# Optimization experiments

Measured on AMD Instinct MI355X. Metric: run time of the kernel, lower is better.

## Reference

```python
import jax, jax.numpy as jnp
import numpy as np

PAD, BOS, EOS, UNK = 0, 1, 2, 3
B, S, V, D, L = 256, 512, 50000, 256, 128

def setup_inputs() -> dict:
    key = jax.random.key(0)
    ks = jax.random.split(key, 12)
    vocab_tensor = jax.random.randint(ks[0], (B, S), 4, V)
    parent_idx = jax.random.randint(ks[1], (B, S), 0, S)
    pbond = jax.random.randint(ks[2], (B, S), 0, 4)
    bond = jax.random.randint(ks[3], (B, S), 0, 4)
    patom = jax.random.randint(ks[4], (B, S), 0, 16)
    atom = jax.random.randint(ks[5], (B, S), 0, 16)
    btype = jax.random.randint(ks[6], (B, S), 0, 4)
    order_tensor = jnp.stack([parent_idx, pbond, bond, patom, atom, btype], axis=-1)
    lengths = jax.random.randint(ks[7], (B,), 1, S + 1)
    mask_tensor = jnp.arange(S)[None, :] < lengths[:, None]  # ragged prefix masks
    eps = jax.random.normal(ks[8], (B, L), dtype=jnp.float32)
    sc = 1.0 / np.sqrt(D)
    emb = jax.random.normal(ks[9], (V, D), dtype=jnp.float32) * sc
    Wm = jax.random.normal(ks[10], (D, L), dtype=jnp.float32) * sc
    Wv = jax.random.normal(ks[11], (D, L), dtype=jnp.float32) * sc
    Wlin = jax.random.normal(jax.random.fold_in(key, 20), (L, D), dtype=jnp.float32) / np.sqrt(L)
    Wout = jax.random.normal(jax.random.fold_in(key, 21), (D, D), dtype=jnp.float32) * sc
    return {
        'vocab_tensor': vocab_tensor, 'order_tensor': order_tensor, 'mask_tensor': mask_tensor,
        'eps': eps, 'emb': emb, 'Wm': Wm, 'bm': jnp.zeros((L,), jnp.float32),
        'Wv': Wv, 'bv': jnp.zeros((L,), jnp.float32), 'Wlin': Wlin,
        'blin': jnp.zeros((D,), jnp.float32), 'Wout': Wout, 'bout': jnp.zeros((D,), jnp.float32),
    }

def _forward(vocab_tensor, order_tensor, mask_tensor, eps, emb, Wm, bm, Wv, bv, Wlin, blin, Wout, bout):
    # --- mask bond-pos columns (torch.where assignments, vectorized) ---
    # (columns 1 and 2 set to -1 where masked; kept implicitly via vt/pad handling)
    # --- calc_chem_z path: masked vocab, parent gather, edge one-hot ---
    vt = jnp.where(mask_tensor, vocab_tensor, PAD)                      # [B,S]
    vocab_emb = emb[vt]                                                 # [B,S,D]
    oi = order_tensor[..., 0]
    oi = jnp.where(oi == -1, BOS, oi)
    parent = jnp.where(mask_tensor, jnp.take_along_axis(vt, oi, axis=1), PAD)
    parent = parent.at[:, 0].set(BOS)
    parent_emb = emb[parent]                                            # [B,S,D]
    idx = jnp.clip(order_tensor[..., 5] - 1, -1, None)
    edge_type = jnp.where((idx >= 0)[..., None],
                          jax.nn.one_hot(jnp.clip(idx, 0), 3, dtype=jnp.float32), 0.0)  # [B,S,3]
    # pooling stand-in for (undefined) StructureEncoder -> [B,D]
    m = mask_tensor[..., None].astype(jnp.float32)
    enc = ((vocab_emb + parent_emb) * m).sum(1) / jnp.maximum(m.sum(1), 1.0)
    enc = enc * (1.0 + 0.0 * edge_type.sum())  # keep edge_type in graph
    # --- LatentSampler ---
    mean = enc @ Wm + bm
    log_var = enc @ Wv + bv
    z = mean + eps * jnp.exp(0.5 * log_var)
    memory = z @ Wlin + blin                                            # [B,D]
    # --- vectorized bos/eos/pad sequence assembly (the hot loop in torch) ---
    inp = jnp.concatenate([jnp.full((B, 1), BOS, vocab_tensor.dtype), vocab_tensor], axis=1)  # [B,S+1]
    mask_ex = jnp.concatenate([jnp.ones((B, 1), bool), mask_tensor], axis=1)
    tgt = jnp.roll(inp, -1, axis=1)
    first_false = jnp.argmax(~mask_ex, axis=1)                          # first eos position
    has_false = jnp.any(~mask_ex, axis=1)
    pos = jnp.arange(S + 1)[None, :]
    tgt = jnp.where(has_false[:, None] & (pos == first_false[:, None] - 1), EOS, tgt)
    kill = has_false[:, None] & (pos >= first_false[:, None])
    tgt = jnp.where(kill, PAD, tgt)
    inp = jnp.where(kill, PAD, inp)
    # edge_index assembly (faithful, consumed by decoder in original)
    padneg = jnp.full((B, 1), -1, order_tensor.dtype)
    edge_index = jnp.concatenate([padneg, jnp.where(mask_tensor, order_tensor[..., 0], -2) + 1], axis=1)
    # --- embedding lookups + decoder stand-in + output head ---
    node_embed = emb[inp]                                               # [B,S+1,D]
    dec = node_embed + memory[:, None, :]
    dec = dec + 0.0 * edge_index[..., None].astype(jnp.float32)         # keep edge_index in graph
    word_emb = dec @ Wout + bout
    tgt_emb = emb[tgt]
    valid = (tgt != PAD)
    sq = (word_emb - tgt_emb) ** 2 * valid[..., None]
    token_loss = sq.sum() / jnp.maximum(valid.sum() * D, 1).astype(jnp.float32)
    kl = -0.5 * jnp.sum(1.0 + log_var - mean ** 2 - jnp.exp(log_var)) / B
    return token_loss, kl

def reference(vocab_tensor, order_tensor, mask_tensor, eps, emb, Wm, bm, Wv, bv, Wlin, blin, Wout, bout):
    return _forward(vocab_tensor, order_tensor, mask_tensor, eps, emb, Wm, bm, Wv, bv, Wlin, blin, Wout, bout)
```

## Files before the change

kernel.cpp:

```cpp
#include <hip/hip_runtime.h>

#define B_ 256
#define S_ 512
#define V_ 50000
#define D_ 256
#define L_ 128
#define NPK 64
#define NSP2 4
#define NLB (B_ * NSP2)

typedef __attribute__((ext_vector_type(8))) short short8;
typedef __attribute__((ext_vector_type(4))) float floatx4;

#define OFF_SQP 16
#define OFF_KL  (OFF_SQP + NLB)
#define OFF_CNT (OFF_KL + 256)
#define OFF_Q   (OFF_CNT + 256)
#define OFF_WB  (OFF_Q + B_ * D_)

__device__ __forceinline__ unsigned short f2bf(float x) {
    unsigned u = __float_as_uint(x);
    u += 0x7FFFu + ((u >> 16) & 1u);
    return (unsigned short)(u >> 16);
}
__device__ __forceinline__ float bf2f(unsigned short u) {
    return __uint_as_float(((unsigned)u) << 16);
}

__global__ __launch_bounds__(256) void enc1(
    const int* __restrict__ vocab, const int* __restrict__ order,
    const int* __restrict__ mask, const float* __restrict__ emb,
    const float* __restrict__ eps, const float* __restrict__ Wm,
    const float* __restrict__ bm, const float* __restrict__ Wv,
    const float* __restrict__ bv, const float* __restrict__ Wlin,
    const float* __restrict__ blin, const float* __restrict__ Wout,
    const float* __restrict__ bout, float* __restrict__ ws) {
    __shared__ __align__(16) char smem[11904];
    const int tid = threadIdx.x;
    if (blockIdx.x < NPK) {
        unsigned short* __restrict__ Wb = (unsigned short*)(ws + OFF_WB);
        const int t = blockIdx.x * 256 + tid;
        const int idx0 = t * 4;
        const int kk = idx0 >> 13;
        const int col = (idx0 >> 5) & 255;
        const int hi = (idx0 >> 3) & 3;
        const int e0 = idx0 & 7;
        const int kbase = kk * 32 + hi * 8 + e0;
        ushort4 h;
        h.x = f2bf(Wout[(size_t)(kbase + 0) * D_ + col]);
        h.y = f2bf(Wout[(size_t)(kbase + 1) * D_ + col]);
        h.z = f2bf(Wout[(size_t)(kbase + 2) * D_ + col]);
        h.w = f2bf(Wout[(size_t)(kbase + 3) * D_ + col]);
        ((ushort4*)Wb)[t] = h;
        return;
    }
    int* s_id1 = (int*)smem;
    int* s_id2 = s_id1 + S_;
    float4* s_part = (float4*)(smem + 4096);
    float* s_enc = (float*)(smem + 7168);
    float* s_mean = (float*)(smem + 8192);
    float* s_lv = (float*)(smem + 8704);
    float* s_z = (float*)(smem + 9216);
    float* s_mem = (float*)(smem + 9728);
    float* s_red = (float*)(smem + 10752);
    int* s_cntp = (int*)(smem + 11776);
    const int b = blockIdx.x - NPK;
    if (tid == 0) *s_cntp = 0;
    __syncthreads();
    for (int j = tid; j < S_; j += 256) {
        const int mk = mask[b * S_ + j];
        int id1 = 0, id2 = 0;
        if (mk) {
            id1 = vocab[b * S_ + j];
            if (j == 0) {
                id2 = 1;
            } else {
                int oi = order[(size_t)(b * S_ + j) * 6];
                if (oi == -1) oi = 1;
                id2 = mask[b * S_ + oi] ? vocab[b * S_ + oi] : 0;
            }
        }
        s_id1[j] = id1;
        s_id2[j] = id2;
        unsigned long long bal = __ballot(mk != 0);
        if ((tid & 63) == 0) atomicAdd(s_cntp, __popcll(bal));
    }
    __syncthreads();
    const int cnt = *s_cntp;
    const int jg = tid >> 6, d4 = tid & 63;
    const float4* eb4 = (const float4*)emb;
    float4 a = {0.f, 0.f, 0.f, 0.f};
#pragma unroll 4
    for (int j = jg; j < cnt; j += 4) {
        float4 x = eb4[(size_t)s_id1[j] * 64 + d4];
        float4 y = eb4[(size_t)s_id2[j] * 64 + d4];
        a.x += x.x + y.x; a.y += x.y + y.y;
        a.z += x.z + y.z; a.w += x.w + y.w;
    }
    if (jg) s_part[(jg - 1) * 64 + d4] = a;
    __syncthreads();
    if (jg == 0) {
#pragma unroll
        for (int g = 0; g < 3; ++g) {
            float4 p = s_part[g * 64 + d4];
            a.x += p.x; a.y += p.y; a.z += p.z; a.w += p.w;
        }
        const float inv = 1.f / fmaxf((float)cnt, 1.f);
        a.x *= inv; a.y *= inv; a.z *= inv; a.w *= inv;
        ((float4*)s_enc)[d4] = a;
    }
    __syncthreads();
    {
        const int l = tid & (L_ - 1);
        const float* W = (tid < L_) ? Wm : Wv;
        const float* bb = (tid < L_) ? bm : bv;
        float dot = bb[l];
        for (int d = 0; d < D_; ++d) dot = fmaf(s_enc[d], W[d * L_ + l], dot);
        if (tid < L_) s_mean[l] = dot; else s_lv[l] = dot;
    }
    __syncthreads();
    float klp = 0.f;
    if (tid < L_) {
        float mn = s_mean[tid], lv = s_lv[tid];
        s_z[tid] = mn + eps[b * L_ + tid] * expf(0.5f * lv);
        klp = 1.f + lv - mn * mn - expf(lv);
    }
    s_red[tid] = klp;
    __syncthreads();
    for (int s = 128; s > 0; s >>= 1) {
        if (tid < s) s_red[tid] += s_red[tid + s];
        __syncthreads();
    }
    if (tid == 0) {
        ws[OFF_KL + b] = s_red[0];
        ((int*)ws)[OFF_CNT + b] = cnt;
    }
    {
        float mem = blin[tid];
        for (int l2 = 0; l2 < L_; ++l2) mem = fmaf(s_z[l2], Wlin[l2 * D_ + tid], mem);
        s_mem[tid] = mem;
    }
    __syncthreads();
    {
        float qv = bout[tid];
        for (int k = 0; k < D_; ++k) qv = fmaf(s_mem[k], Wout[k * D_ + tid], qv);
        ws[OFF_Q + b * D_ + tid] = qv;
    }
}

__global__ __launch_bounds__(256, 2) void loss2(const int* __restrict__ vocab,
                                                const float* __restrict__ emb,
                                                float* __restrict__ ws) {
    __shared__ __align__(16) char smemA[8192];
    __shared__ __align__(16) float smemT[16 * 260];
    __shared__ int s_tgt[16];
    __shared__ float s_w[16];
    __shared__ int s_inp0;
    __shared__ float s_q[256];
    __shared__ float s_wred[4];
    const int tid = threadIdx.x;
    const int b = blockIdx.x >> 2, part = blockIdx.x & 3;
    const int lane = tid & 63, wv = tid >> 6;
    const int lo = lane & 15, hi = lane >> 4;
    const unsigned short* __restrict__ Wb = (const unsigned short*)(ws + OFF_WB);
    const int cnt = ((const int*)ws)[OFF_CNT + b];
    const int ntiles = (cnt + 16) >> 4;
    s_q[tid] = ws[OFF_Q + b * D_ + tid];
    short8 bfr[4][8];
#pragma unroll
    for (int nt = 0; nt < 4; ++nt)
#pragma unroll
        for (int kk = 0; kk < 8; ++kk)
            bfr[nt][kk] = *(const short8*)(Wb + kk * 8192 +
                                           (wv * 64 + nt * 16 + lo) * 32 + hi * 8);
    float sqacc = 0.f;
    for (int ti = part; ti < ntiles; ti += NSP2) {
        if (tid < 16) {
            const int j = ti * 16 + tid;
            s_tgt[tid] = (j < cnt) ? vocab[b * S_ + j] : ((cnt < S_) ? 2 : 1);
            s_w[tid] = (j <= cnt) ? 1.f : 0.f;
            if (tid == 0) s_inp0 = (ti == 0) ? 1 : vocab[b * S_ + ti * 16 - 1];
        }
        __syncthreads();
#pragma unroll
        for (int i = 0; i < 4; ++i) {
            const int fi = i * 256 + tid;
            const int row = fi >> 6, cf4 = fi & 63;
            float4 t = *((const float4*)(emb + (size_t)s_tgt[row] * D_) + cf4);
            *(float4*)(&smemT[row * 260 + cf4 * 4]) = t;
            if (row < 15) {
                const int arow = row + 1;
                ushort4 h;
                h.x = f2bf(t.x); h.y = f2bf(t.y); h.z = f2bf(t.z); h.w = f2bf(t.w);
                const int byt = (arow * 512 + cf4 * 8) ^ ((arow & 7) << 4);
                *(ushort4*)(smemA + byt) = h;
            }
        }
        if (tid < 64) {
            float4 v = *((const float4*)(emb + (size_t)s_inp0 * D_) + tid);
            ushort4 h;
            h.x = f2bf(v.x); h.y = f2bf(v.y); h.z = f2bf(v.z); h.w = f2bf(v.w);
            *(ushort4*)(smemA + tid * 8) = h;
        }
        __syncthreads();
        floatx4 acc[4];
#pragma unroll
        for (int nt = 0; nt < 4; ++nt) acc[nt] = (floatx4){0.f, 0.f, 0.f, 0.f};
#pragma unroll
        for (int kk = 0; kk < 8; ++kk) {
            const int byt = (lo * 512 + hi * 16 + kk * 64) ^ ((lo & 7) << 4);
            short8 av = *(const short8*)(smemA + byt);
#pragma unroll
            for (int nt = 0; nt < 4; ++nt)
                acc[nt] = __builtin_amdgcn_mfma_f32_16x16x32_bf16(
                    av, bfr[nt][kk], acc[nt], 0, 0, 0);
        }
#pragma unroll
        for (int nt = 0; nt < 4; ++nt) {
            const int col = wv * 64 + nt * 16 + lo;
            const float qv = s_q[col];
#pragma unroll
            for (int r = 0; r < 4; ++r) {
                const int row = hi * 4 + r;
                const float t = smemT[row * 260 + col];
                const float d = acc[nt][r] + qv - t;
                sqacc = fmaf(s_w[row] * d, d, sqacc);
            }
        }
        __syncthreads();
    }
#pragma unroll
    for (int off = 32; off; off >>= 1) sqacc += __shfl_down(sqacc, off, 64);
    if (lane == 0) s_wred[wv] = sqacc;
    __syncthreads();
    if (tid == 0)
        ws[OFF_SQP + blockIdx.x] = s_wred[0] + s_wred[1] + s_wred[2] + s_wred[3];
}

__global__ __launch_bounds__(256) void finalize3(const float* __restrict__ ws,
                                                 float* __restrict__ out) {
    __shared__ float s_red[256];
    const int tid = threadIdx.x;
    float sq = 0.f;
#pragma unroll
    for (int i = 0; i < NSP2; ++i) sq += ws[OFF_SQP + i * 256 + tid];
    s_red[tid] = sq;
    __syncthreads();
    for (int s = 128; s > 0; s >>= 1) {
        if (tid < s) s_red[tid] += s_red[tid + s];
        __syncthreads();
    }
    const float sq_tot = s_red[0];
    __syncthreads();
    s_red[tid] = ws[OFF_KL + tid];
    __syncthreads();
    for (int s = 128; s > 0; s >>= 1) {
        if (tid < s) s_red[tid] += s_red[tid + s];
        __syncthreads();
    }
    const float kl_tot = s_red[0];
    __syncthreads();
    s_red[tid] = (float)(((const int*)ws)[OFF_CNT + tid] + 1);
    __syncthreads();
    for (int s = 128; s > 0; s >>= 1) {
        if (tid < s) s_red[tid] += s_red[tid + s];
        __syncthreads();
    }
    if (tid == 0) {
        float denom = s_red[0] * (float)D_;
        if (denom < 1.f) denom = 1.f;
        out[0] = sq_tot / denom;
        out[1] = -0.5f * kl_tot / (float)B_;
    }
}

extern "C" void kernel_launch(void* const* d_in, const int* in_sizes, int n_in,
                              void* d_out, int out_size, void* d_ws, size_t ws_size,
                              hipStream_t stream) {
    const int* vocab = (const int*)d_in[0];
    const int* order = (const int*)d_in[1];
    const int* mask  = (const int*)d_in[2];
    const float* eps  = (const float*)d_in[3];
    const float* emb  = (const float*)d_in[4];
    const float* Wm   = (const float*)d_in[5];
    const float* bm   = (const float*)d_in[6];
    const float* Wv   = (const float*)d_in[7];
    const float* bv   = (const float*)d_in[8];
    const float* Wlin = (const float*)d_in[9];
    const float* blin = (const float*)d_in[10];
    const float* Wout = (const float*)d_in[11];
    const float* bout = (const float*)d_in[12];

    float* ws = (float*)d_ws;
    enc1<<<NPK + B_, 256, 0, stream>>>(vocab, order, mask, emb, eps, Wm, bm,
                                       Wv, bv, Wlin, blin, Wout, bout, ws);
    loss2<<<NLB, 256, 0, stream>>>(vocab, emb, ws);
    finalize3<<<1, 256, 0, stream>>>(ws, (float*)d_out);
}
```

Before: 181.9 us.

## Prefetch next tile's embeddings into registers and split tiles contiguously per block

Each block now takes a contiguous range of tiles instead of a strided one, and loads that range's vocab ids into shared memory once. While the MFMA work runs on the current tile, the embedding rows for the next tile are loaded into registers, which hides global gather latency behind compute. The row weights are computed inline and one barrier per iteration is dropped. The grid mapping is also reordered so that consecutive blocks belong to different batches, not to the same batch. The register prefetch raises register pressure under launch bounds of 2 blocks per SM.

```diff
diff --git a/kernel.cpp b/kernel.cpp
--- a/kernel.cpp
+++ b/kernel.cpp
@@ -153,18 +153,28 @@
                                                 float* __restrict__ ws) {
     __shared__ __align__(16) char smemA[8192];
     __shared__ __align__(16) float smemT[16 * 260];
-    __shared__ int s_tgt[16];
-    __shared__ float s_w[16];
-    __shared__ int s_inp0;
+    __shared__ int s_sid[160];
     __shared__ float s_q[256];
     __shared__ float s_wred[4];
     const int tid = threadIdx.x;
-    const int b = blockIdx.x >> 2, part = blockIdx.x & 3;
+    const int b = blockIdx.x & (B_ - 1), part = blockIdx.x >> 8;
     const int lane = tid & 63, wv = tid >> 6;
     const int lo = lane & 15, hi = lane >> 4;
     const unsigned short* __restrict__ Wb = (const unsigned short*)(ws + OFF_WB);
     const int cnt = ((const int*)ws)[OFF_CNT + b];
     const int ntiles = (cnt + 16) >> 4;
+    const int per16 = (ntiles + NSP2 - 1) / NSP2;
+    const int tb = part * per16;
+    const int te = min(tb + per16, ntiles);
+    if (tb >= te) {
+        if (tid == 0) ws[OFF_SQP + blockIdx.x] = 0.f;
+        return;
+    }
+    const int ecode = (cnt < S_) ? 2 : 1;
+    const int jlo = (tb > 0) ? tb * 16 - 1 : 0;
+    const int jhi = min(te * 16, cnt);
+    const int len = jhi - jlo;
+    if (tid < len) s_sid[tid] = vocab[b * S_ + jlo + tid];
     s_q[tid] = ws[OFF_Q + b * D_ + tid];
     short8 bfr[4][8];
 #pragma unroll
@@ -173,36 +183,61 @@
         for (int kk = 0; kk < 8; ++kk)
             bfr[nt][kk] = *(const short8*)(Wb + kk * 8192 +
                                            (wv * 64 + nt * 16 + lo) * 32 + hi * 8);
+    __syncthreads();
+    const int srow = tid >> 6;
+    const int scf4 = tid & 63;
+    float4 RT[4];
+    float4 RA0 = {0.f, 0.f, 0.f, 0.f};
+#pragma unroll
+    for (int i = 0; i < 4; ++i) {
+        const int row = srow + i * 4;
+        const int j = tb * 16 + row;
+        const int id = (j < cnt) ? s_sid[j - jlo] : ecode;
+        RT[i] = *((const float4*)(emb + (size_t)id * D_) + scf4);
+    }
+    if (tid < 64) {
+        const int j0 = tb * 16;
+        const int aid = (j0 == 0) ? 1 : s_sid[j0 - 1 - jlo];
+        RA0 = *((const float4*)(emb + (size_t)aid * D_) + tid);
+    }
     float sqacc = 0.f;
-    for (int ti = part; ti < ntiles; ti += NSP2) {
-        if (tid < 16) {
-            const int j = ti * 16 + tid;
-            s_tgt[tid] = (j < cnt) ? vocab[b * S_ + j] : ((cnt < S_) ? 2 : 1);
-            s_w[tid] = (j <= cnt) ? 1.f : 0.f;
-            if (tid == 0) s_inp0 = (ti == 0) ? 1 : vocab[b * S_ + ti * 16 - 1];
-        }
+    for (int t = tb; t < te; ++t) {
         __syncthreads();
 #pragma unroll
         for (int i = 0; i < 4; ++i) {
-            const int fi = i * 256 + tid;
-            const int row = fi >> 6, cf4 = fi & 63;
-            float4 t = *((const float4*)(emb + (size_t)s_tgt[row] * D_) + cf4);
-            *(float4*)(&smemT[row * 260 + cf4 * 4]) = t;
+            const int row = srow + i * 4;
+            *(float4*)(&smemT[row * 260 + scf4 * 4]) = RT[i];
             if (row < 15) {
                 const int arow = row + 1;
                 ushort4 h;
-                h.x = f2bf(t.x); h.y = f2bf(t.y); h.z = f2bf(t.z); h.w = f2bf(t.w);
-                const int byt = (arow * 512 + cf4 * 8) ^ ((arow & 7) << 4);
+                h.x = f2bf(RT[i].x); h.y = f2bf(RT[i].y);
+                h.z = f2bf(RT[i].z); h.w = f2bf(RT[i].w);
+                const int byt = (arow * 512 + scf4 * 8) ^ ((arow & 7) << 4);
                 *(ushort4*)(smemA + byt) = h;
             }
         }
         if (tid < 64) {
-            float4 v = *((const float4*)(emb + (size_t)s_inp0 * D_) + tid);
             ushort4 h;
-            h.x = f2bf(v.x); h.y = f2bf(v.y); h.z = f2bf(v.z); h.w = f2bf(v.w);
+            h.x = f2bf(RA0.x); h.y = f2bf(RA0.y);
+            h.z = f2bf(RA0.z); h.w = f2bf(RA0.w);
             *(ushort4*)(smemA + tid * 8) = h;
         }
         __syncthreads();
+        float4 RTn[4] = {RT[0], RT[1], RT[2], RT[3]};
+        float4 RA0n = RA0;
+        if (t + 1 < te) {
+#pragma unroll
+            for (int i = 0; i < 4; ++i) {
+                const int row = srow + i * 4;
+                const int j = (t + 1) * 16 + row;
+                const int id = (j < cnt) ? s_sid[j - jlo] : ecode;
+                RTn[i] = *((const float4*)(emb + (size_t)id * D_) + scf4);
+            }
+            if (tid < 64) {
+                const int aid = s_sid[(t + 1) * 16 - 1 - jlo];
+                RA0n = *((const float4*)(emb + (size_t)aid * D_) + tid);
+            }
+        }
         floatx4 acc[4];
 #pragma unroll
         for (int nt = 0; nt < 4; ++nt) acc[nt] = (floatx4){0.f, 0.f, 0.f, 0.f};
@@ -222,12 +257,15 @@
 #pragma unroll
             for (int r = 0; r < 4; ++r) {
                 const int row = hi * 4 + r;
-                const float t = smemT[row * 260 + col];
-                const float d = acc[nt][r] + qv - t;
-                sqacc = fmaf(s_w[row] * d, d, sqacc);
-            }
-        }
-        __syncthreads();
+                const float w = (t * 16 + row <= cnt) ? 1.f : 0.f;
+                const float tv = smemT[row * 260 + col];
+                const float d = acc[nt][r] + qv - tv;
+                sqacc = fmaf(w * d, d, sqacc);
+            }
+        }
+#pragma unroll
+        for (int i = 0; i < 4; ++i) RT[i] = RTn[i];
+        RA0 = RA0n;
     }
 #pragma unroll
     for (int off = 32; off; off >>= 1) sqacc += __shfl_down(sqacc, off, 64);
```

Result: faster. 162.1 us (-10.9%).
